# Kernel tuning notes

Measured on AMD Instinct MI355X. Metric: run time of the kernel, lower is better.

The kernel has to match this reference:

```python
import jax, jax.numpy as jnp
import numpy as np

NUM_CLASS = 20
STRIDE = 4.0
B, H, W, G, NV = 8, 128, 128, 64, 40


def setup_inputs() -> dict:
    key = jax.random.key(0)
    ks = jax.random.split(key, 8)
    keypoints = jax.random.normal(ks[0], (B, H, W, NUM_CLASS), jnp.float32)
    preg = jax.random.uniform(ks[1], (B, H, W, 4), jnp.float32, 1.0, 40.0)
    fpn = jax.random.normal(ks[2], (B, H, W, NUM_CLASS), jnp.float32)
    masks = jnp.ones((B, H, W, G), jnp.float32)
    scalar_y = jax.random.uniform(ks[3], (B, G), jnp.float32, 5.0, 25.0)
    scalar_x = jax.random.uniform(ks[4], (B, G), jnp.float32, 5.0, 25.0)
    # ground truth: [cy, cx, y1, x1, y2, x2, class]; rows >= NV are zero padding
    rng = np.random.default_rng(0)
    gt = np.zeros((B, G, 7), np.float32)
    cy = rng.uniform(20.0, 492.0, (B, NV)).astype(np.float32)
    cx = rng.uniform(20.0, 492.0, (B, NV)).astype(np.float32)
    hh = rng.uniform(16.0, 120.0, (B, NV)).astype(np.float32)
    ww = rng.uniform(16.0, 120.0, (B, NV)).astype(np.float32)
    gt[:, :NV, 0] = cy
    gt[:, :NV, 1] = cx
    gt[:, :NV, 2] = np.clip(cy - hh / 2, 1.0, 510.0)
    gt[:, :NV, 3] = np.clip(cx - ww / 2, 1.0, 510.0)
    gt[:, :NV, 4] = np.clip(cy + hh / 2, 1.0, 510.0)
    gt[:, :NV, 5] = np.clip(cx + ww / 2, 1.0, 510.0)
    gt[:, :NV, 6] = rng.integers(1, NUM_CLASS + 1, (B, NV)).astype(np.float32)
    return {
        "keypoints": keypoints,
        "preg": preg,
        "fpn": fpn,
        "ground_truth": jnp.asarray(gt),
        "masks": masks,
        "scalar_y": scalar_y,
        "scalar_x": scalar_x,
    }


def _image_loss(gravity_pred, dist_pred, heatmap_pred, gt, masks, sy, sx):
    f32 = jnp.float32
    Hh, Ww, C = gravity_pred.shape
    Gg = gt.shape[0]
    # padding boundary: first row whose cy (col 0) is the minimum (==0 padding)
    slice_index = jnp.argmin(gt[:, 0])
    valid = jnp.arange(Gg) < slice_index
    vf = valid.astype(f32)

    gy = (gt[:, 0] + 0.5) / STRIDE
    gx = (gt[:, 1] + 0.5) / STRIDE
    by1 = (gt[:, 2] + 0.5) / STRIDE
    bx1 = (gt[:, 3] + 0.5) / STRIDE
    by2 = (gt[:, 4] + 0.5) / STRIDE
    bx2 = (gt[:, 5] + 0.5) / STRIDE
    cid = gt[:, 6].astype(jnp.int32) - 1
    kp_y = jnp.clip(jnp.floor(gt[:, 0] / STRIDE).astype(jnp.int32), 0, Hh - 1)
    kp_x = jnp.clip(jnp.floor(gt[:, 1] / STRIDE).astype(jnp.int32), 0, Ww - 1)

    grid_y = (jnp.arange(Hh, dtype=f32) + 0.5)[:, None, None]  # [H,1,1]
    grid_x = (jnp.arange(Ww, dtype=f32) + 0.5)[None, :, None]  # [1,W,1]

    dist_l = grid_x - bx1  # [1,W,G]
    dist_r = bx2 - grid_x
    dist_t = grid_y - by1  # [H,1,G]
    dist_b = by2 - grid_y
    ymask = (dist_t > 0.0).astype(f32) * (dist_b > 0.0).astype(f32)
    xmask = (dist_l > 0.0).astype(f32) * (dist_r > 0.0).astype(f32)
    heatmask = ymask * xmask * masks * vf  # [H,W,G]
    dist_l = dist_l * heatmask
    dist_r = dist_r * heatmask
    dist_t = dist_t * heatmask
    dist_b = dist_b * heatmask
    loc = jnp.max(heatmask, axis=-1)  # [H,W]
    dist_area = (dist_l + dist_r) * (dist_t + dist_b)
    area_pad = dist_area + (1.0 - heatmask) * 1e8
    area_min = jnp.min(area_pad, axis=-1, keepdims=True)
    dist_mask = (dist_area == area_min).astype(f32) * loc[..., None]  # [H,W,G]
    dl = jnp.max(dist_l * dist_mask, axis=-1)
    dr = jnp.max(dist_r * dist_mask, axis=-1)
    dt = jnp.max(dist_t * dist_mask, axis=-1)
    db = jnp.max(dist_b * dist_mask, axis=-1)

    pl, pr, pt, pb = (dist_pred[..., k] for k in range(4))
    inter = (jnp.minimum(dl, pl) + jnp.minimum(dr, pr)) * (jnp.minimum(dt, pt) + jnp.minimum(db, pb))
    union = (dl + dr) * (dt + db) + (pl + pr) * (pt + pb) - inter
    iou = inter / (union + 1e-12)

    red = jnp.exp(-(((grid_y - 0.5 - jnp.floor(gy)) / jnp.sqrt(sy)) ** 2
                    + ((grid_x - 0.5 - jnp.floor(gx)) / jnp.sqrt(sx)) ** 2) / 2.0) * vf  # [H,W,G]
    iou_red = jnp.max(red, axis=-1)
    iou_loss = jnp.sum(-jnp.log(iou + 1e-12) * loc * (iou_red * 4.0 + 1.0))

    # per-class max over gts of that class (== boolean_mask + reduce_max; empty -> 0)
    seg = jnp.where(valid & (cid >= 0) & (cid < C), cid, C)
    red_gt = jnp.maximum(jax.ops.segment_max(red.transpose(2, 0, 1), seg, num_segments=C + 1)[:C], 0.0).transpose(1, 2, 0)
    hm_gt = jnp.maximum(jax.ops.segment_max(dist_mask.transpose(2, 0, 1), seg, num_segments=C + 1)[:C], 0.0).transpose(1, 2, 0)
    gt_kp = jnp.zeros((Hh, Ww, C + 1), f32).at[kp_y, kp_x, seg].max(vf)[..., :C]

    sig, ls = jax.nn.sigmoid, jax.nn.log_sigmoid
    pos = -(1.0 - sig(gravity_pred)) ** 2 * ls(gravity_pred) * gt_kp
    neg = -(1.0 - red_gt) ** 4 * sig(gravity_pred) ** 2 * (-gravity_pred + ls(gravity_pred)) * (1.0 - gt_kp)
    gravity_loss = jnp.sum(pos) + jnp.sum(neg)

    hpos = -10.0 * (1.0 - sig(heatmap_pred)) ** 2 * ls(heatmap_pred) * hm_gt
    hneg = -10.0 * sig(heatmap_pred) ** 2 * (-heatmap_pred + ls(heatmap_pred)) * (1.0 - hm_gt)
    s_hg = jnp.sum(hm_gt)
    hm_loss = jnp.sum(hneg) / (jnp.asarray(Hh * Ww * C, f32) - s_hg)

    cond = s_hg != 0.0
    safe_hg = jnp.where(cond, s_hg, 1.0)
    s_loc = jnp.sum(loc)
    safe_loc = jnp.where(s_loc > 0.0, s_loc, 1.0)
    n_valid = jnp.maximum(slice_index.astype(f32), 1.0)
    hm2 = hm_loss + jnp.sum(hpos) / safe_hg
    iou_out = jnp.where(cond, iou_loss / safe_loc, 0.0)
    grav_out = jnp.where(cond, gravity_loss / n_valid, 0.0)
    hm_out = jnp.where(cond, hm2, hm_loss)
    total = jnp.where(cond, iou_out + grav_out + hm2, hm_loss)
    return iou_out, hm_out, grav_out, total


def reference(keypoints, preg, fpn, ground_truth, masks, scalar_y, scalar_x):
    losses = jax.vmap(_image_loss)(keypoints, preg, fpn, ground_truth, masks, scalar_y, scalar_x)
    # layer returns the mean total loss over the batch
    return jnp.mean(losses[3])
```

## Files before the change

### kernel.cpp

```cpp
#include <hip/hip_runtime.h>
#include <math.h>

#define Bc 8
#define Hc 128
#define Wc 128
#define Cc 20
#define Gc 64
#define HWc (Hc*Wc)
#define NBLK (Bc*HWc/256)

#define WS_STRIDE 768
#define OFF_BOX   0
#define OFF_RED   256
#define OFF_KPIX  512
#define OFF_SEG   576
#define OFF_START 640
#define WS_NV     704
#define WS_ACC    705
#define WS_SLICE  712

__global__ __launch_bounds__(64) void prep_kernel(
    const float* __restrict__ gt, const float* __restrict__ sy,
    const float* __restrict__ sx, float* __restrict__ ws)
{
  const int b = blockIdx.x;
  const int g = threadIdx.x;
  const float* row = gt + (size_t)(b*Gc + g)*7;
  const float cy = row[0];
  const float cx = row[1];

  float v = cy; int idx = g;
  #pragma unroll
  for (int o = 32; o > 0; o >>= 1) {
    const float ov = __shfl_down(v, o, 64);
    const int   oi = __shfl_down(idx, o, 64);
    if (ov < v || (ov == v && oi < idx)) { v = ov; idx = oi; }
  }
  const int slice = __shfl(idx, 0, 64);
  const bool valid = g < slice;
  const int cid = (int)row[6] - 1;
  const int cls = (cid >= 0 && cid < Cc) ? cid : Cc;

  __shared__ int counts[Cc+1], offs[Cc+1], starts[Cc+2];
  if (g < Cc+1) { counts[g] = 0; offs[g] = 0; }
  __syncthreads();
  if (valid) atomicAdd(&counts[cls], 1);
  __syncthreads();
  if (g == 0) {
    int acc = 0;
    for (int c = 0; c < Cc+1; ++c) { starts[c] = acc; acc += counts[c]; }
    starts[Cc+1] = acc;
  }
  __syncthreads();

  float* wb = ws + (size_t)b*WS_STRIDE;
  int*  wbi = (int*)wb;
  float4 bx;
  bx.x = (row[2]+0.5f)*0.25f;
  bx.y = (row[3]+0.5f)*0.25f;
  bx.z = (row[4]+0.5f)*0.25f;
  bx.w = (row[5]+0.5f)*0.25f;
  ((float4*)(wb + OFF_BOX))[g] = bx;
  wbi[OFF_SEG+g] = (valid && cls < Cc) ? cls : Cc;
  if (valid) {
    const int pos = starts[cls] + atomicAdd(&offs[cls], 1);
    float4 rp;
    rp.x = floorf((cy+0.5f)*0.25f);
    rp.y = floorf((cx+0.5f)*0.25f);
    rp.z = 1.0f / sy[b*Gc+g];
    rp.w = 1.0f / sx[b*Gc+g];
    ((float4*)(wb + OFF_RED))[pos] = rp;
    int kpy = (int)floorf(cy*0.25f); kpy = kpy < 0 ? 0 : (kpy > Hc-1 ? Hc-1 : kpy);
    int kpx = (int)floorf(cx*0.25f); kpx = kpx < 0 ? 0 : (kpx > Wc-1 ? Wc-1 : kpx);
    wbi[OFF_KPIX+pos] = kpy*Wc + kpx;
  }
  if (g < Cc+2) wbi[OFF_START+g] = starts[g];
  if (g == 0) { wb[WS_NV] = fmaxf((float)slice, 1.0f); wbi[WS_SLICE] = slice; }
  if (g < 6) wb[WS_ACC+g] = 0.0f;
}

__device__ __forceinline__ float wave_sum(float v) {
  #pragma unroll
  for (int o = 32; o > 0; o >>= 1) v += __shfl_down(v, o, 64);
  return v;
}

__global__ __launch_bounds__(256) void main_kernel(
  const float* __restrict__ kpt, const float* __restrict__ preg,
  const float* __restrict__ fpn, const float* __restrict__ masks,
  const float* __restrict__ wsc, float* __restrict__ wsa)
{
  __shared__ float s_part[4][6];

  const int tid = threadIdx.x;
  const int b   = blockIdx.x >> 6;
  const int pix = blockIdx.x*256 + tid;
  const int hw  = pix & (HWc-1);
  const int h = hw >> 7, w = hw & (Wc-1);

  const float* wb  = wsc + (size_t)b*WS_STRIDE;
  const int*   wbi = (const int*)wb;
  const float4* __restrict__ box4 = (const float4*)(wb + OFF_BOX);
  const float4* __restrict__ red4 = (const float4*)(wb + OFF_RED);
  const int nslice = wbi[WS_SLICE];

  const float wx = w + 0.5f, hy = h + 0.5f;
  const float px_ = (float)w, py_ = (float)h;
  const float4* mrow4 = (const float4*)(masks + (size_t)pix*Gc);
  const float4 p4 = *(const float4*)(preg + (size_t)pix*4);

  float amin = 3.0e38f; float loc = 0.0f; int gmin = 0;
  #pragma unroll
  for (int g0 = 0; g0 < Gc; g0 += 4) {
    float4 m4 = make_float4(0.f, 0.f, 0.f, 0.f);
    if (g0 < nslice) m4 = mrow4[g0 >> 2];
    #pragma unroll
    for (int j = 0; j < 4; ++j) {
      const int g = g0 + j;
      const float m = (j==0) ? m4.x : (j==1) ? m4.y : (j==2) ? m4.z : m4.w;
      const float4 bx = box4[g];
      const float dl = wx - bx.y, dr = bx.w - wx;
      const float dt = hy - bx.x, db = bx.z - hy;
      const bool inb = (dl > 0.f) & (dr > 0.f) & (dt > 0.f) & (db > 0.f) && (g < nslice);
      const float hm = inb ? m : 0.f;
      const float area = (dl*hm + dr*hm) * (dt*hm + db*hm);
      const float ap = area + (1.f - hm)*1e8f;
      if (ap < amin) { amin = ap; gmin = g; }
      loc = fmaxf(loc, hm);
    }
  }

  const float4* kq4 = (const float4*)(kpt + (size_t)pix*Cc);
  const float4* fq4 = (const float4*)(fpn + (size_t)pix*Cc);
  float kf[Cc], ff[Cc];
  #pragma unroll
  for (int t = 0; t < 5; ++t) {
    const float4 a = kq4[t], c = fq4[t];
    kf[4*t]=a.x; kf[4*t+1]=a.y; kf[4*t+2]=a.z; kf[4*t+3]=a.w;
    ff[4*t]=c.x; ff[4*t+1]=c.y; ff[4*t+2]=c.z; ff[4*t+3]=c.w;
  }

  float dlm=0.f, drm=0.f, dtm=0.f, dbm=0.f, hmval=0.f; int cmin = Cc;
  if (loc > 0.f) {
    const float m = masks[(size_t)pix*Gc + gmin];
    const float4 bx = box4[gmin];
    const float dl = wx - bx.y, dr = bx.w - wx;
    const float dt = hy - bx.x, db = bx.z - hy;
    const float area = (dl*m + dr*m) * (dt*m + db*m);
    if (area == amin) {
      dlm = dl*m*loc; drm = dr*m*loc; dtm = dt*m*loc; dbm = db*m*loc;
      cmin = wbi[OFF_SEG + gmin];
      hmval = loc;
    }
  }

  float iou_red = 0.f, grav = 0.f, hneg = 0.f;
  int s0 = wbi[OFF_START];
  #pragma unroll
  for (int c = 0; c < Cc; ++c) {
    const int s1 = wbi[OFF_START + c + 1];
    float rmax = 0.f; bool kpv = false;
    for (int i = s0; i < s1; ++i) {
      const float4 rp = red4[i];
      const int kpix = wbi[OFF_KPIX + i];
      const float dy = py_ - rp.x, dx = px_ - rp.y;
      const float red = __expf(-0.5f*(dy*dy*rp.z + dx*dx*rp.w));
      iou_red = fmaxf(iou_red, red);
      rmax = fmaxf(rmax, red);
      kpv = kpv | (kpix == hw);
    }
    s0 = s1;
    const float x  = kf[c];
    const float e  = __expf(-fabsf(x));
    const float t  = 1.f + e;
    const float r  = 1.f / t;
    const float L  = __logf(t);
    const float s  = (x >= 0.f) ? r : e*r;
    const float lsx = fminf(x, 0.f) - L;
    const float kv = kpv ? 1.f : 0.f;
    const float om = 1.f - rmax;
    const float om4 = (om*om)*(om*om);
    const float oms = 1.f - s;
    grav += (-(oms*oms)*lsx)*kv + (-om4*(s*s)*(lsx - x))*(1.f - kv);

    const float fx  = ff[c];
    const float ef  = __expf(-fabsf(fx));
    const float tf  = 1.f + ef;
    const float rf  = 1.f / tf;
    const float Lf  = __logf(tf);
    const float sf  = (fx >= 0.f) ? rf : ef*rf;
    const float lsf = fminf(fx, 0.f) - Lf;
    hneg += -10.f*(sf*sf)*(lsf - fx);
  }
  {
    const int e20 = wbi[OFF_START + Cc + 1];
    for (int i = s0; i < e20; ++i) {
      const float4 rp = red4[i];
      const float dy = py_ - rp.x, dx = px_ - rp.y;
      iou_red = fmaxf(iou_red, __expf(-0.5f*(dy*dy*rp.z + dx*dx*rp.w)));
    }
  }

  const float inter = (fminf(dlm,p4.x)+fminf(drm,p4.y)) * (fminf(dtm,p4.z)+fminf(dbm,p4.w));
  const float uni = (dlm+drm)*(dtm+dbm) + (p4.x+p4.y)*(p4.z+p4.w) - inter;
  const float iou = inter / (uni + 1e-12f);
  const float t_iou = -__logf(iou + 1e-12f) * loc * (iou_red*4.f + 1.f);

  float hpos = 0.f, shg = 0.f;
  if (hmval > 0.f && cmin < Cc) {
    float fx = 0.f;
    #pragma unroll
    for (int c = 0; c < Cc; ++c) if (c == cmin) fx = ff[c];
    const float ef  = __expf(-fabsf(fx));
    const float tf  = 1.f + ef;
    const float rf  = 1.f / tf;
    const float Lf  = __logf(tf);
    const float sf  = (fx >= 0.f) ? rf : ef*rf;
    const float lsf = fminf(fx, 0.f) - Lf;
    const float osf = 1.f - sf;
    hpos = -10.f*(osf*osf)*lsf*hmval;
    hneg -= (-10.f*(sf*sf)*(lsf - fx))*hmval;
    shg = hmval;
  }

  float v0 = wave_sum(t_iou);
  float v1 = wave_sum(loc);
  float v2 = wave_sum(grav);
  float v3 = wave_sum(hpos);
  float v4 = wave_sum(hneg);
  float v5 = wave_sum(shg);
  const int wv = tid >> 6, ln = tid & 63;
  if (ln == 0) {
    s_part[wv][0]=v0; s_part[wv][1]=v1; s_part[wv][2]=v2;
    s_part[wv][3]=v3; s_part[wv][4]=v4; s_part[wv][5]=v5;
  }
  __syncthreads();
  if (tid < 6) {
    const float a = s_part[0][tid] + s_part[1][tid] + s_part[2][tid] + s_part[3][tid];
    atomicAdd(wsa + (size_t)b*WS_STRIDE + WS_ACC + tid, a);
  }
}

__global__ __launch_bounds__(64) void fin_kernel(const float* __restrict__ ws,
                                                 float* __restrict__ out)
{
  const int b = threadIdx.x;
  float total = 0.0f;
  if (b < Bc) {
    const float* wb = ws + (size_t)b*WS_STRIDE;
    const float iou_loss = wb[WS_ACC+0];
    const float s_loc    = wb[WS_ACC+1];
    const float grav     = wb[WS_ACC+2];
    const float hposs    = wb[WS_ACC+3];
    const float hnegs    = wb[WS_ACC+4];
    const float shg      = wb[WS_ACC+5];
    const float nv       = wb[WS_NV];
    const float hm_loss  = hnegs / ((float)(HWc*Cc) - shg);
    const bool  cond     = (shg != 0.0f);
    const float safe_hg  = cond ? shg : 1.0f;
    const float safe_loc = (s_loc > 0.0f) ? s_loc : 1.0f;
    const float hm2      = hm_loss + hposs/safe_hg;
    total = cond ? (iou_loss/safe_loc + grav/nv + hm2) : hm_loss;
  }
  #pragma unroll
  for (int o = 4; o > 0; o >>= 1) total += __shfl_down(total, o, 64);
  if (b == 0) out[0] = total * (1.0f/(float)Bc);
}

extern "C" void kernel_launch(void* const* d_in, const int* in_sizes, int n_in,
                              void* d_out, int out_size, void* d_ws, size_t ws_size,
                              hipStream_t stream) {
  const float* kpt  = (const float*)d_in[0];
  const float* preg = (const float*)d_in[1];
  const float* fpn  = (const float*)d_in[2];
  const float* gt   = (const float*)d_in[3];
  const float* mk   = (const float*)d_in[4];
  const float* sy   = (const float*)d_in[5];
  const float* sx   = (const float*)d_in[6];
  float* ws  = (float*)d_ws;
  float* out = (float*)d_out;

  prep_kernel<<<Bc, 64, 0, stream>>>(gt, sy, sx, ws);
  main_kernel<<<NBLK, 256, 0, stream>>>(kpt, preg, fpn, mk, ws, ws);
  fin_kernel<<<1, 64, 0, stream>>>(ws, out);
}
```

Before: 138.1 us.

## Cut register pressure in main kernel by streaming class inputs and bounding occupancy

The kernel no longer keeps the 40 keypoint and heatmap values per pixel in registers. It loads each float4 group just before the per-class loop uses it, and re-reads the single fpn value at cmin from global memory. The mask loop now runs only up to the valid-object count, eight objects per iteration, instead of a fully unrolled 64-iteration loop. `__launch_bounds__(256, 4)` asks the compiler for enough occupancy to fit four blocks per CU. The goal is lower VGPR use and more waves to hide latency, at the cost of less unrolling, loop overhead and possible spills if the occupancy target forces them.

```diff
diff --git a/kernel.cpp b/kernel.cpp
--- a/kernel.cpp
+++ b/kernel.cpp
@@ -85,7 +85,7 @@
   return v;
 }
 
-__global__ __launch_bounds__(256) void main_kernel(
+__global__ __launch_bounds__(256, 4) void main_kernel(
   const float* __restrict__ kpt, const float* __restrict__ preg,
   const float* __restrict__ fpn, const float* __restrict__ masks,
   const float* __restrict__ wsc, float* __restrict__ wsa)
@@ -110,14 +110,14 @@
   const float4 p4 = *(const float4*)(preg + (size_t)pix*4);
 
   float amin = 3.0e38f; float loc = 0.0f; int gmin = 0;
-  #pragma unroll
-  for (int g0 = 0; g0 < Gc; g0 += 4) {
-    float4 m4 = make_float4(0.f, 0.f, 0.f, 0.f);
-    if (g0 < nslice) m4 = mrow4[g0 >> 2];
+  for (int g0 = 0; g0 < nslice; g0 += 8) {
+    const float4 ma = mrow4[(g0 >> 2)];
+    const float4 mb = mrow4[(g0 >> 2) + 1];
     #pragma unroll
-    for (int j = 0; j < 4; ++j) {
+    for (int j = 0; j < 8; ++j) {
       const int g = g0 + j;
-      const float m = (j==0) ? m4.x : (j==1) ? m4.y : (j==2) ? m4.z : m4.w;
+      const float m = (j==0)?ma.x:(j==1)?ma.y:(j==2)?ma.z:(j==3)?ma.w
+                    : (j==4)?mb.x:(j==5)?mb.y:(j==6)?mb.z:mb.w;
       const float4 bx = box4[g];
       const float dl = wx - bx.y, dr = bx.w - wx;
       const float dt = hy - bx.x, db = bx.z - hy;
@@ -128,16 +128,6 @@
       if (ap < amin) { amin = ap; gmin = g; }
       loc = fmaxf(loc, hm);
     }
-  }
-
-  const float4* kq4 = (const float4*)(kpt + (size_t)pix*Cc);
-  const float4* fq4 = (const float4*)(fpn + (size_t)pix*Cc);
-  float kf[Cc], ff[Cc];
-  #pragma unroll
-  for (int t = 0; t < 5; ++t) {
-    const float4 a = kq4[t], c = fq4[t];
-    kf[4*t]=a.x; kf[4*t+1]=a.y; kf[4*t+2]=a.z; kf[4*t+3]=a.w;
-    ff[4*t]=c.x; ff[4*t+1]=c.y; ff[4*t+2]=c.z; ff[4*t+3]=c.w;
   }
 
   float dlm=0.f, drm=0.f, dtm=0.f, dbm=0.f, hmval=0.f; int cmin = Cc;
@@ -154,43 +144,50 @@
     }
   }
 
+  const float4* kq4 = (const float4*)(kpt + (size_t)pix*Cc);
+  const float4* fq4 = (const float4*)(fpn + (size_t)pix*Cc);
   float iou_red = 0.f, grav = 0.f, hneg = 0.f;
   int s0 = wbi[OFF_START];
-  #pragma unroll
-  for (int c = 0; c < Cc; ++c) {
-    const int s1 = wbi[OFF_START + c + 1];
-    float rmax = 0.f; bool kpv = false;
-    for (int i = s0; i < s1; ++i) {
-      const float4 rp = red4[i];
-      const int kpix = wbi[OFF_KPIX + i];
-      const float dy = py_ - rp.x, dx = px_ - rp.y;
-      const float red = __expf(-0.5f*(dy*dy*rp.z + dx*dx*rp.w));
-      iou_red = fmaxf(iou_red, red);
-      rmax = fmaxf(rmax, red);
-      kpv = kpv | (kpix == hw);
-    }
-    s0 = s1;
-    const float x  = kf[c];
-    const float e  = __expf(-fabsf(x));
-    const float t  = 1.f + e;
-    const float r  = 1.f / t;
-    const float L  = __logf(t);
-    const float s  = (x >= 0.f) ? r : e*r;
-    const float lsx = fminf(x, 0.f) - L;
-    const float kv = kpv ? 1.f : 0.f;
-    const float om = 1.f - rmax;
-    const float om4 = (om*om)*(om*om);
-    const float oms = 1.f - s;
-    grav += (-(oms*oms)*lsx)*kv + (-om4*(s*s)*(lsx - x))*(1.f - kv);
-
-    const float fx  = ff[c];
-    const float ef  = __expf(-fabsf(fx));
-    const float tf  = 1.f + ef;
-    const float rf  = 1.f / tf;
-    const float Lf  = __logf(tf);
-    const float sf  = (fx >= 0.f) ? rf : ef*rf;
-    const float lsf = fminf(fx, 0.f) - Lf;
-    hneg += -10.f*(sf*sf)*(lsf - fx);
+  for (int cg = 0; cg < 5; ++cg) {
+    const float4 kv4 = kq4[cg];
+    const float4 fv4 = fq4[cg];
+    #pragma unroll
+    for (int j = 0; j < 4; ++j) {
+      const int c = cg*4 + j;
+      const int s1 = wbi[OFF_START + c + 1];
+      float rmax = 0.f; bool kpv = false;
+      for (int i = s0; i < s1; ++i) {
+        const float4 rp = red4[i];
+        const int kpix = wbi[OFF_KPIX + i];
+        const float dy = py_ - rp.x, dx = px_ - rp.y;
+        const float red = __expf(-0.5f*(dy*dy*rp.z + dx*dx*rp.w));
+        iou_red = fmaxf(iou_red, red);
+        rmax = fmaxf(rmax, red);
+        kpv = kpv | (kpix == hw);
+      }
+      s0 = s1;
+      const float x  = (j==0)?kv4.x:(j==1)?kv4.y:(j==2)?kv4.z:kv4.w;
+      const float e  = __expf(-fabsf(x));
+      const float t  = 1.f + e;
+      const float r  = 1.f / t;
+      const float L  = __logf(t);
+      const float s  = (x >= 0.f) ? r : e*r;
+      const float lsx = fminf(x, 0.f) - L;
+      const float kv = kpv ? 1.f : 0.f;
+      const float om = 1.f - rmax;
+      const float om4 = (om*om)*(om*om);
+      const float oms = 1.f - s;
+      grav += (-(oms*oms)*lsx)*kv + (-om4*(s*s)*(lsx - x))*(1.f - kv);
+
+      const float fx  = (j==0)?fv4.x:(j==1)?fv4.y:(j==2)?fv4.z:fv4.w;
+      const float ef  = __expf(-fabsf(fx));
+      const float tf  = 1.f + ef;
+      const float rf  = 1.f / tf;
+      const float Lf  = __logf(tf);
+      const float sf  = (fx >= 0.f) ? rf : ef*rf;
+      const float lsf = fminf(fx, 0.f) - Lf;
+      hneg += -10.f*(sf*sf)*(lsf - fx);
+    }
   }
   {
     const int e20 = wbi[OFF_START + Cc + 1];
@@ -208,9 +205,7 @@
 
   float hpos = 0.f, shg = 0.f;
   if (hmval > 0.f && cmin < Cc) {
-    float fx = 0.f;
-    #pragma unroll
-    for (int c = 0; c < Cc; ++c) if (c == cmin) fx = ff[c];
+    const float fx  = fpn[(size_t)pix*Cc + cmin];
     const float ef  = __expf(-fabsf(fx));
     const float tf  = 1.f + ef;
     const float rf  = 1.f / tf;
```

Result: faster. 117.1 us (-15.2%).
